# Performance work log

Measured on AMD Instinct MI355X. Metric: run time of the kernel, lower is better.

The kernel has to match this reference:

```python
import jax, jax.numpy as jnp
from jax import lax
import numpy as np

B, C, H, W = 4, 256, 64, 64
CQK = C // 8  # 32


def conv3x3(x, w, b):
    # x: [B,C_in,H,W], w: [C_out,C_in,3,3], b: [C_out]
    y = lax.conv_general_dilated(x, w, window_strides=(1, 1), padding='SAME',
                                 dimension_numbers=('NCHW', 'OIHW', 'NCHW'))
    return y + b[None, :, None, None]


def setup_inputs() -> dict:
    key = jax.random.key(0)
    ks = jax.random.split(key, 8)
    scale = 0.02
    return {
        'x': jax.random.normal(ks[0], (B, C, H, W), dtype=jnp.float32),
        'wq': jax.random.normal(ks[1], (CQK, C, 3, 3), dtype=jnp.float32) * scale,
        'bq': jax.random.normal(ks[2], (CQK,), dtype=jnp.float32) * scale,
        'wk': jax.random.normal(ks[3], (CQK, C, 3, 3), dtype=jnp.float32) * scale,
        'bk': jax.random.normal(ks[4], (CQK,), dtype=jnp.float32) * scale,
        'wv': jax.random.normal(ks[5], (C, C, 3, 3), dtype=jnp.float32) * scale,
        'bv': jax.random.normal(ks[6], (C,), dtype=jnp.float32) * scale,
        'gamma': jax.random.normal(ks[7], (1,), dtype=jnp.float32) * scale,
    }


def reference(x, wq, bq, wk, bk, wv, bv, gamma):
    b, c, h, w = x.shape
    n = h * w
    # Q: [B, N, C//8]  (permute(0,2,1) of the flattened conv output)
    q = conv3x3(x, wq, bq).reshape(b, -1, n).transpose(0, 2, 1)
    # K: [B, C//8, N]
    k = conv3x3(x, wk, bk).reshape(b, -1, n)
    # s: [B, N_q, N_k]
    s = jnp.einsum('bqd,bdk->bqk', q, k)
    # NOTE: original uses Softmax(dim=-2), i.e. over the QUERY axis
    attn_T = jax.nn.softmax(s, axis=-2)
    # V: [B, C, N]
    v = conv3x3(x, wv, bv).reshape(b, c, n)
    # o = bmm(V, attn_T): [B, C, N]
    o = jnp.einsum('bcq,bqk->bck', v, attn_T).reshape(b, c, h, w)
    return x + gamma * o
```

## Files before the change

kernel.cpp:

```cpp
#include <hip/hip_runtime.h>
#include <cstddef>

#define N_PIX 4096
#define HW 64
#define LOG2E 1.4426950408889634f
#define SHIFT2 28.8539008177793f

typedef __attribute__((ext_vector_type(8))) short bf16x8;
typedef __attribute__((ext_vector_type(4))) float f32x4;
typedef unsigned int u32;

static __device__ __forceinline__ unsigned short f2bf(float f) {
    union { float f; unsigned u; } v; v.f = f;
    unsigned r = v.u + 0x7fffu + ((v.u >> 16) & 1u);
    return (unsigned short)(r >> 16);
}
static __device__ __forceinline__ float bf2f(unsigned short s) {
    union { unsigned u; float f; } v; v.u = (unsigned)s << 16;
    return v.f;
}
static __device__ __forceinline__ unsigned pack_bf16_trunc(float lo, float hi) {
    union { float f; unsigned u; } a, b; a.f = hi; b.f = lo;
    return __builtin_amdgcn_perm(a.u, b.u, 0x07060302u);
}
static __device__ __forceinline__ void gll16(const void* g, void* l) {
    __builtin_amdgcn_global_load_lds(
        (const __attribute__((address_space(1))) u32*)g,
        (__attribute__((address_space(3))) u32*)l, 16, 0, 0);
}

__global__ __launch_bounds__(256) void x_transpose(
    const float* __restrict__ x, unsigned short* __restrict__ xbf)
{
    __shared__ unsigned short Ts[64][72];
    const int tid = threadIdx.x;
    const int px0 = blockIdx.x * 64, ci0 = blockIdx.y * 64, b = blockIdx.z;
    const float* xb = x + ((size_t)b * 256 + ci0) * N_PIX;

#pragma unroll
    for (int r = 0; r < 4; ++r) {
        int c = r * 16 + (tid >> 4);
        int p4 = (tid & 15) * 4;
        float4 v = *(const float4*)&xb[(size_t)c * N_PIX + px0 + p4];
        Ts[c][p4 + 0] = f2bf(v.x);
        Ts[c][p4 + 1] = f2bf(v.y);
        Ts[c][p4 + 2] = f2bf(v.z);
        Ts[c][p4 + 3] = f2bf(v.w);
    }
    __syncthreads();
#pragma unroll
    for (int r = 0; r < 2; ++r) {
        int id = tid * 2 + r;
        int p = id >> 3, c8 = (id & 7) * 8;
        ushort4 lo, hi;
        lo.x = Ts[c8 + 0][p]; lo.y = Ts[c8 + 1][p];
        lo.z = Ts[c8 + 2][p]; lo.w = Ts[c8 + 3][p];
        hi.x = Ts[c8 + 4][p]; hi.y = Ts[c8 + 5][p];
        hi.z = Ts[c8 + 6][p]; hi.w = Ts[c8 + 7][p];
        size_t off = ((size_t)b * N_PIX + px0 + p) * 256 + ci0 + c8;
        *(ushort4*)&xbf[off]     = lo;
        *(ushort4*)&xbf[off + 4] = hi;
    }
}

__global__ __launch_bounds__(256) void w_transform(
    const float* __restrict__ wq, const float* __restrict__ wk,
    const float* __restrict__ wv, unsigned short* __restrict__ wAll,
    unsigned short* __restrict__ zp)
{
    int gid = blockIdx.x * 256 + threadIdx.x;
    if (gid < 256) zp[gid] = 0;
    if (gid >= 72 * 320 * 4) return;
    int part = gid & 3;
    int m = (gid >> 2) % 320;
    int kb = gid / 1280;
    int t = kb >> 3;
    int ci0 = (kb & 7) * 32 + part * 8;
    const float* src; int co; float sc = 1.f;
    if (m < 256)      { src = wv; co = m; }
    else if (m < 288) { src = wq; co = m - 256; sc = LOG2E; }
    else              { src = wk; co = m - 288; }
    ushort4 lo, hi;
    lo.x = f2bf(sc * src[((size_t)co * 256 + ci0 + 0) * 9 + t]);
    lo.y = f2bf(sc * src[((size_t)co * 256 + ci0 + 1) * 9 + t]);
    lo.z = f2bf(sc * src[((size_t)co * 256 + ci0 + 2) * 9 + t]);
    lo.w = f2bf(sc * src[((size_t)co * 256 + ci0 + 3) * 9 + t]);
    hi.x = f2bf(sc * src[((size_t)co * 256 + ci0 + 4) * 9 + t]);
    hi.y = f2bf(sc * src[((size_t)co * 256 + ci0 + 5) * 9 + t]);
    hi.z = f2bf(sc * src[((size_t)co * 256 + ci0 + 6) * 9 + t]);
    hi.w = f2bf(sc * src[((size_t)co * 256 + ci0 + 7) * 9 + t]);
    size_t off = ((size_t)kb * 320 + m) * 32 + part * 8;
    *(ushort4*)&wAll[off]     = lo;
    *(ushort4*)&wAll[off + 4] = hi;
}

__global__ __launch_bounds__(256, 2) void conv_gemm_v6(
    const unsigned short* __restrict__ xbf, const unsigned short* __restrict__ wAll,
    const float* __restrict__ bq, const float* __restrict__ bk,
    const float* __restrict__ bv, const unsigned short* __restrict__ zpage,
    unsigned short* __restrict__ vbf, unsigned short* __restrict__ qt,
    unsigned short* __restrict__ kt)
{
    __shared__ unsigned short Bl[3 * 7168];

    const int tid = threadIdx.x;
    const int w = tid >> 6, lane = tid & 63, quad = lane >> 4, l15 = lane & 15;
    const int y = blockIdx.x, rh = blockIdx.y, b = blockIdx.z;
    const int rg = w >> 1;
    const int pxh = w & 1;

    const unsigned short* xb = xbf + (size_t)b * N_PIX * 256;
    const unsigned short* aSrc = wAll + (size_t)rh * 160 * 32;

    auto stage = [&](int kb, int buf) {
        const int t_ = kb >> 3;
        const int ty = t_ / 3;
        const int dy = ty - 1, dx = t_ - ty * 3 - 1;
        const int gy = y + dy;
        const bool rowOK = ((unsigned)gy < 64u);
        const int ci0 = (kb & 7) * 32;
        const unsigned short* aS = aSrc + (size_t)kb * 10240;
        unsigned short* tile = &Bl[buf * 7168];
#pragma unroll
        for (int r = 0; r < 4; ++r) {
            const int c = r * 4 + w;
            if (r == 3 && w >= 2) continue;
            if (c < 10) {
                int o = c * 1024 + lane * 16;
                int u = o ^ (((o >> 7) & 7) << 4);
                gll16(aS + (u >> 1), tile + c * 512);
            } else {
                int o = (c - 10) * 1024 + lane * 16;
                int u = o ^ (((o >> 7) & 7) << 4);
                int px = u >> 6, k16 = (u >> 4) & 3;
                int gx = px + dx;
                const unsigned short* src =
                    (rowOK && (unsigned)gx < 64u)
                        ? xb + ((size_t)(gy * 64 + gx) * 256 + ci0 + k16 * 8)
                        : zpage;
                gll16(src, tile + 5120 + (c - 10) * 512);
            }
        }
    };

    f32x4 acc[5][2];
#pragma unroll
    for (int cb = 0; cb < 5; ++cb)
#pragma unroll
        for (int jb = 0; jb < 2; ++jb) acc[cb][jb] = (f32x4){0.f, 0.f, 0.f, 0.f};

    stage(0, 0);
    stage(1, 1);
    if (w < 2) asm volatile("s_waitcnt vmcnt(4)" ::: "memory");
    else       asm volatile("s_waitcnt vmcnt(3)" ::: "memory");
    __builtin_amdgcn_s_barrier();
    __builtin_amdgcn_sched_barrier(0);

    int buf = 0;
    for (int kb = 0; kb < 72; ++kb) {
        int nb = buf + 1; if (nb == 3) nb = 0;
        int pb = nb + 1;  if (pb == 3) pb = 0;
        const bool more2 = (kb + 2 < 72);
        const bool more1 = (kb + 1 < 72);
        if (more2) stage(kb + 2, pb);

        const int bb = buf * 7168;
        bf16x8 af[5], bfr[2];
#pragma unroll
        for (int cb = 0; cb < 5; ++cb) {
            int sr = rg * 80 + cb * 16 + l15;
            int u = sr * 64 + quad * 16;
            u ^= ((u >> 7) & 7) << 4;
            af[cb] = *(const bf16x8*)&Bl[bb + (u >> 1)];
        }
#pragma unroll
        for (int jb = 0; jb < 2; ++jb) {
            int px = pxh * 32 + jb * 16 + l15;
            int u = px * 64 + quad * 16;
            u ^= ((u >> 7) & 7) << 4;
            bfr[jb] = *(const bf16x8*)&Bl[bb + 5120 + (u >> 1)];
        }
        __builtin_amdgcn_s_setprio(1);
#pragma unroll
        for (int cb = 0; cb < 5; ++cb)
#pragma unroll
            for (int jb = 0; jb < 2; ++jb)
                acc[cb][jb] = __builtin_amdgcn_mfma_f32_16x16x32_bf16(
                    af[cb], bfr[jb], acc[cb][jb], 0, 0, 0);
        __builtin_amdgcn_s_setprio(0);

        if (more2) {
            if (w < 2) asm volatile("s_waitcnt vmcnt(4)" ::: "memory");
            else       asm volatile("s_waitcnt vmcnt(3)" ::: "memory");
        } else if (more1) {
            asm volatile("s_waitcnt vmcnt(0)" ::: "memory");
        }
        if (more1) {
            __builtin_amdgcn_s_barrier();
            __builtin_amdgcn_sched_barrier(0);
        }
        buf = nb;
    }

#pragma unroll
    for (int cb = 0; cb < 5; ++cb) {
        int cBase = rh * 160 + rg * 80 + cb * 16 + quad * 4;
#pragma unroll
        for (int r = 0; r < 4; ++r) {
            int c = cBase + r;
            if (c < 256) {
                float bias = bv[c];
#pragma unroll
                for (int jb = 0; jb < 2; ++jb) {
                    int px = y * 64 + pxh * 32 + jb * 16 + l15;
                    vbf[((size_t)b * 256 + c) * N_PIX + px] = f2bf(acc[cb][jb][r] + bias);
                }
            } else if (c < 288) {
                float bias = bq[c - 256] * LOG2E;
#pragma unroll
                for (int jb = 0; jb < 2; ++jb) {
                    int px = y * 64 + pxh * 32 + jb * 16 + l15;
                    qt[((size_t)b * N_PIX + px) * 32 + (c - 256)] = f2bf(acc[cb][jb][r] + bias);
                }
            } else {
                float bias = bk[c - 288];
#pragma unroll
                for (int jb = 0; jb < 2; ++jb) {
                    int px = y * 64 + pxh * 32 + jb * 16 + l15;
                    kt[((size_t)b * N_PIX + px) * 32 + (c - 288)] = f2bf(acc[cb][jb][r] + bias);
                }
            }
        }
    }
}

__global__ __launch_bounds__(256, 2) void fused_attn_mfma(
    const unsigned short* __restrict__ qt, const unsigned short* __restrict__ kt,
    const unsigned short* __restrict__ vbf,
    unsigned short* __restrict__ Abuf, float* __restrict__ lbuf, int iRange)
{
    const int tid  = threadIdx.x;
    const int w    = tid >> 6;
    const int lane = tid & 63;
    const int quad = lane >> 4;
    const int l15  = lane & 15;
    const int j0   = blockIdx.x * 128;
    const int b    = blockIdx.y;
    const int sp   = blockIdx.z;
    const int iBeg = sp * iRange;
    const int NI   = iRange / 64;

    const unsigned short* qtb = qt + (size_t)b * N_PIX * 32;
    const unsigned short* ktb = kt + (size_t)b * N_PIX * 32;
    const unsigned short* vb  = vbf + (size_t)b * 256 * N_PIX;

    __shared__ unsigned Pfrag[2][4096];
    __shared__ float lred[4][128];

    bf16x8 kf[8];
#pragma unroll
    for (int jb = 0; jb < 8; ++jb)
        kf[jb] = *(const bf16x8*)&ktb[((size_t)(j0 + jb * 16 + l15)) * 32 + quad * 8];

    f32x4 acc[4][8];
#pragma unroll
    for (int cb = 0; cb < 4; ++cb)
#pragma unroll
        for (int jb = 0; jb < 8; ++jb)
            acc[cb][jb] = (f32x4){0.f, 0.f, 0.f, 0.f};

    float lpart[8] = {0.f, 0.f, 0.f, 0.f, 0.f, 0.f, 0.f, 0.f};

    const int wFrag = w >> 1;
    const int wL    = ((w & 1) << 5) + ((quad >> 1) << 4) + l15;
    const int wEl2  = (quad & 1) << 1;

    bf16x8 va[2][4];

    auto s_phase = [&](bf16x8 qa, int buf) {
#pragma unroll
        for (int jb = 0; jb < 8; ++jb) {
            f32x4 s = __builtin_amdgcn_mfma_f32_16x16x32_bf16(
                qa, kf[jb], (f32x4){-SHIFT2, -SHIFT2, -SHIFT2, -SHIFT2}, 0, 0, 0);
            float p0 = __builtin_amdgcn_exp2f(s[0]);
            float p1 = __builtin_amdgcn_exp2f(s[1]);
            float p2 = __builtin_amdgcn_exp2f(s[2]);
            float p3 = __builtin_amdgcn_exp2f(s[3]);
            lpart[jb] += (p0 + p1) + (p2 + p3);
            unsigned u0 = pack_bf16_trunc(p0, p1);
            unsigned u1 = pack_bf16_trunc(p2, p3);
            unsigned base = (((jb << 1) + wFrag) * 64 + wL) * 4 + wEl2;
            Pfrag[buf][base]     = u0;
            Pfrag[buf][base + 1] = u1;
        }
    };

    auto load_qa = [&](int i0) {
        return *(const bf16x8*)&qtb[((size_t)(i0 + w * 16 + l15)) * 32 + quad * 8];
    };
    auto load_va = [&](int i0) {
#pragma unroll
        for (int ks = 0; ks < 2; ++ks)
#pragma unroll
            for (int cb = 0; cb < 4; ++cb)
                va[ks][cb] = *(const bf16x8*)&vb[((size_t)(w * 64 + cb * 16 + l15)) * N_PIX
                                                 + i0 + ks * 32 + quad * 8];
    };

    load_va(iBeg);
    s_phase(load_qa(iBeg), 0);

    for (int n = 0; n < NI; ++n) {
        __syncthreads();
        const bool hasN = (n + 1 < NI);
        const int inext = iBeg + (n + 1) * 64;
        bf16x8 qaN;
        if (hasN) qaN = load_qa(inext);

#pragma unroll
        for (int ks = 0; ks < 2; ++ks) {
            bf16x8 pb[8];
#pragma unroll
            for (int jb = 0; jb < 8; ++jb)
                pb[jb] = *(const bf16x8*)&Pfrag[n & 1][(((jb << 1) + ks) * 64 + lane) * 4];
#pragma unroll
            for (int cb = 0; cb < 4; ++cb)
#pragma unroll
                for (int jb = 0; jb < 8; ++jb)
                    acc[cb][jb] = __builtin_amdgcn_mfma_f32_16x16x32_bf16(
                        va[ks][cb], pb[jb], acc[cb][jb], 0, 0, 0);
        }

        if (hasN) {
            load_va(inext);
            s_phase(qaN, (n + 1) & 1);
        }
    }

#pragma unroll
    for (int jb = 0; jb < 8; ++jb) {
        float v = lpart[jb];
        v += __shfl_xor(v, 16, 64);
        v += __shfl_xor(v, 32, 64);
        lpart[jb] = v;
    }
    if (lane < 16) {
#pragma unroll
        for (int jb = 0; jb < 8; ++jb)
            lred[w][jb * 16 + l15] = lpart[jb];
    }
    __syncthreads();
    if (tid < 128) {
        float s = lred[0][tid] + lred[1][tid] + lred[2][tid] + lred[3][tid];
        lbuf[((size_t)sp * 4 + b) * N_PIX + j0 + tid] = s;
    }

    unsigned short* Ab = Abuf + ((size_t)sp * 4 + b) * 256 * N_PIX;
#pragma unroll
    for (int cb = 0; cb < 4; ++cb) {
        int c = w * 64 + cb * 16 + quad * 4;
#pragma unroll
        for (int jb = 0; jb < 8; ++jb) {
            int j = j0 + jb * 16 + l15;
#pragma unroll
            for (int r = 0; r < 4; ++r)
                Ab[(size_t)(c + r) * N_PIX + j] = f2bf(acc[cb][jb][r]);
        }
    }
}

__global__ __launch_bounds__(256) void combine_kernel(
    const unsigned short* __restrict__ A, const float* __restrict__ L,
    const float* __restrict__ x, const float* __restrict__ gamma,
    float* __restrict__ out, int split)
{
    const size_t CH = (size_t)4 * 256 * N_PIX;
    size_t flat = ((size_t)blockIdx.x * 256 + threadIdx.x) * 8;
    int j = (int)(flat & (N_PIX - 1));
    int b = (int)(flat >> 20);

    float a[8] = {0.f, 0.f, 0.f, 0.f, 0.f, 0.f, 0.f, 0.f};
    float l[8] = {0.f, 0.f, 0.f, 0.f, 0.f, 0.f, 0.f, 0.f};
    for (int s = 0; s < split; ++s) {
        ushort4 av0 = *(const ushort4*)&A[flat + (size_t)s * CH];
        ushort4 av1 = *(const ushort4*)&A[flat + (size_t)s * CH + 4];
        a[0] += bf2f(av0.x); a[1] += bf2f(av0.y); a[2] += bf2f(av0.z); a[3] += bf2f(av0.w);
        a[4] += bf2f(av1.x); a[5] += bf2f(av1.y); a[6] += bf2f(av1.z); a[7] += bf2f(av1.w);
        float4 l0 = *(const float4*)&L[((size_t)s * 4 + b) * N_PIX + j];
        float4 l1 = *(const float4*)&L[((size_t)s * 4 + b) * N_PIX + j + 4];
        l[0] += l0.x; l[1] += l0.y; l[2] += l0.z; l[3] += l0.w;
        l[4] += l1.x; l[5] += l1.y; l[6] += l1.z; l[7] += l1.w;
    }
    float g = gamma[0];
    float4 x0 = *(const float4*)&x[flat];
    float4 x1 = *(const float4*)&x[flat + 4];
    float4 o0, o1;
    o0.x = x0.x + g * a[0] / l[0];
    o0.y = x0.y + g * a[1] / l[1];
    o0.z = x0.z + g * a[2] / l[2];
    o0.w = x0.w + g * a[3] / l[3];
    o1.x = x1.x + g * a[4] / l[4];
    o1.y = x1.y + g * a[5] / l[5];
    o1.z = x1.z + g * a[6] / l[6];
    o1.w = x1.w + g * a[7] / l[7];
    *(float4*)&out[flat]     = o0;
    *(float4*)&out[flat + 4] = o1;
}

extern "C" void kernel_launch(void* const* d_in, const int* in_sizes, int n_in,
                              void* d_out, int out_size, void* d_ws, size_t ws_size,
                              hipStream_t stream)
{
    const float* x     = (const float*)d_in[0];
    const float* wq    = (const float*)d_in[1];
    const float* bq    = (const float*)d_in[2];
    const float* wk    = (const float*)d_in[3];
    const float* bk    = (const float*)d_in[4];
    const float* wv    = (const float*)d_in[5];
    const float* bv    = (const float*)d_in[6];
    const float* gamma = (const float*)d_in[7];
    float* out = (float*)d_out;

    const size_t szQTel  = (size_t)4 * N_PIX * 32;
    const size_t szVBFel = (size_t)4 * 256 * N_PIX;
    const size_t szXBFel = (size_t)4 * N_PIX * 256;
    const size_t szWel   = (size_t)72 * 320 * 32;
    const size_t fixedB  = (2 * szQTel + szVBFel + szXBFel + szWel + 256) * 2;

    int split = 4;
    while (split > 1) {
        size_t need = fixedB
                    + (size_t)split * 4 * 256 * N_PIX * 2
                    + (size_t)split * 4 * N_PIX * 4;
        if (need <= ws_size) break;
        split >>= 1;
    }

    unsigned short* Abuf = (unsigned short*)d_ws;
    float* lbuf = (float*)(Abuf + (size_t)split * 4 * 256 * N_PIX);
    unsigned short* qt    = (unsigned short*)(lbuf + (size_t)split * 4 * N_PIX);
    unsigned short* kt    = qt + szQTel;
    unsigned short* vbf   = kt + szQTel;
    unsigned short* xbf   = vbf + szVBFel;
    unsigned short* wAll  = xbf + szXBFel;
    unsigned short* zpage = wAll + szWel;

    x_transpose<<<dim3(N_PIX / 64, 4, 4), 256, 0, stream>>>(x, xbf);
    w_transform<<<dim3((72 * 320 * 4 + 255) / 256), 256, 0, stream>>>(
        wq, wk, wv, wAll, zpage);

    conv_gemm_v6<<<dim3(HW, 2, 4), 256, 0, stream>>>(
        xbf, wAll, bq, bk, bv, zpage, vbf, qt, kt);

    fused_attn_mfma<<<dim3(N_PIX / 128, 4, split), 256, 0, stream>>>(
        qt, kt, vbf, Abuf, lbuf, N_PIX / split);

    combine_kernel<<<dim3((4 * 256 * N_PIX) / (256 * 8)), 256, 0, stream>>>(
        Abuf, lbuf, x, gamma, out, split);
}
```

Before: 178.7 us.

## Merge prep kernels, deepen conv pipeline to four stages, raise attention MFMA priority

Combines the x transpose and weight transform into one launch, using an extra grid slice for the weights to save a kernel launch. Deepens the conv GEMM LDS ring from three buffers to four so loads are issued three K-blocks ahead, with vmcnt waits adjusted for each tail stage. Also wraps the attention MFMA loop in s_setprio. The fourth buffer raises LDS use, which may reduce occupancy at two blocks per CU.

```diff
diff --git a/kernel.cpp b/kernel.cpp
--- a/kernel.cpp
+++ b/kernel.cpp
@@ -29,79 +29,82 @@
         (__attribute__((address_space(3))) u32*)l, 16, 0, 0);
 }
 
-__global__ __launch_bounds__(256) void x_transpose(
-    const float* __restrict__ x, unsigned short* __restrict__ xbf)
-{
-    __shared__ unsigned short Ts[64][72];
-    const int tid = threadIdx.x;
-    const int px0 = blockIdx.x * 64, ci0 = blockIdx.y * 64, b = blockIdx.z;
-    const float* xb = x + ((size_t)b * 256 + ci0) * N_PIX;
-
-#pragma unroll
-    for (int r = 0; r < 4; ++r) {
-        int c = r * 16 + (tid >> 4);
-        int p4 = (tid & 15) * 4;
-        float4 v = *(const float4*)&xb[(size_t)c * N_PIX + px0 + p4];
-        Ts[c][p4 + 0] = f2bf(v.x);
-        Ts[c][p4 + 1] = f2bf(v.y);
-        Ts[c][p4 + 2] = f2bf(v.z);
-        Ts[c][p4 + 3] = f2bf(v.w);
-    }
-    __syncthreads();
-#pragma unroll
-    for (int r = 0; r < 2; ++r) {
-        int id = tid * 2 + r;
-        int p = id >> 3, c8 = (id & 7) * 8;
-        ushort4 lo, hi;
-        lo.x = Ts[c8 + 0][p]; lo.y = Ts[c8 + 1][p];
-        lo.z = Ts[c8 + 2][p]; lo.w = Ts[c8 + 3][p];
-        hi.x = Ts[c8 + 4][p]; hi.y = Ts[c8 + 5][p];
-        hi.z = Ts[c8 + 6][p]; hi.w = Ts[c8 + 7][p];
-        size_t off = ((size_t)b * N_PIX + px0 + p) * 256 + ci0 + c8;
-        *(ushort4*)&xbf[off]     = lo;
-        *(ushort4*)&xbf[off + 4] = hi;
-    }
-}
-
-__global__ __launch_bounds__(256) void w_transform(
+__global__ __launch_bounds__(256) void prep_kernel(
+    const float* __restrict__ x, unsigned short* __restrict__ xbf,
     const float* __restrict__ wq, const float* __restrict__ wk,
     const float* __restrict__ wv, unsigned short* __restrict__ wAll,
     unsigned short* __restrict__ zp)
 {
-    int gid = blockIdx.x * 256 + threadIdx.x;
-    if (gid < 256) zp[gid] = 0;
-    if (gid >= 72 * 320 * 4) return;
-    int part = gid & 3;
-    int m = (gid >> 2) % 320;
-    int kb = gid / 1280;
-    int t = kb >> 3;
-    int ci0 = (kb & 7) * 32 + part * 8;
-    const float* src; int co; float sc = 1.f;
-    if (m < 256)      { src = wv; co = m; }
-    else if (m < 288) { src = wq; co = m - 256; sc = LOG2E; }
-    else              { src = wk; co = m - 288; }
-    ushort4 lo, hi;
-    lo.x = f2bf(sc * src[((size_t)co * 256 + ci0 + 0) * 9 + t]);
-    lo.y = f2bf(sc * src[((size_t)co * 256 + ci0 + 1) * 9 + t]);
-    lo.z = f2bf(sc * src[((size_t)co * 256 + ci0 + 2) * 9 + t]);
-    lo.w = f2bf(sc * src[((size_t)co * 256 + ci0 + 3) * 9 + t]);
-    hi.x = f2bf(sc * src[((size_t)co * 256 + ci0 + 4) * 9 + t]);
-    hi.y = f2bf(sc * src[((size_t)co * 256 + ci0 + 5) * 9 + t]);
-    hi.z = f2bf(sc * src[((size_t)co * 256 + ci0 + 6) * 9 + t]);
-    hi.w = f2bf(sc * src[((size_t)co * 256 + ci0 + 7) * 9 + t]);
-    size_t off = ((size_t)kb * 320 + m) * 32 + part * 8;
-    *(ushort4*)&wAll[off]     = lo;
-    *(ushort4*)&wAll[off + 4] = hi;
-}
-
-__global__ __launch_bounds__(256, 2) void conv_gemm_v6(
+    const int tid = threadIdx.x;
+    if (blockIdx.z < 4) {
+        __shared__ unsigned short Ts[64][72];
+        const int px0 = blockIdx.x * 64, ci0 = blockIdx.y * 64, b = blockIdx.z;
+        const float* xb = x + ((size_t)b * 256 + ci0) * N_PIX;
+
+#pragma unroll
+        for (int r = 0; r < 4; ++r) {
+            int c = r * 16 + (tid >> 4);
+            int p4 = (tid & 15) * 4;
+            float4 v = *(const float4*)&xb[(size_t)c * N_PIX + px0 + p4];
+            Ts[c][p4 + 0] = f2bf(v.x);
+            Ts[c][p4 + 1] = f2bf(v.y);
+            Ts[c][p4 + 2] = f2bf(v.z);
+            Ts[c][p4 + 3] = f2bf(v.w);
+        }
+        __syncthreads();
+#pragma unroll
+        for (int r = 0; r < 2; ++r) {
+            int id = tid * 2 + r;
+            int p = id >> 3, c8 = (id & 7) * 8;
+            ushort4 lo, hi;
+            lo.x = Ts[c8 + 0][p]; lo.y = Ts[c8 + 1][p];
+            lo.z = Ts[c8 + 2][p]; lo.w = Ts[c8 + 3][p];
+            hi.x = Ts[c8 + 4][p]; hi.y = Ts[c8 + 5][p];
+            hi.z = Ts[c8 + 6][p]; hi.w = Ts[c8 + 7][p];
+            size_t off = ((size_t)b * N_PIX + px0 + p) * 256 + ci0 + c8;
+            *(ushort4*)&xbf[off]     = lo;
+            *(ushort4*)&xbf[off + 4] = hi;
+        }
+    } else {
+        const int f = blockIdx.y * 64 + blockIdx.x;
+#pragma unroll
+        for (int base = 0; base < 2; ++base) {
+            int gid = base * 65536 + f * 256 + tid;
+            if (gid < 256) zp[gid] = 0;
+            if (gid >= 72 * 320 * 4) continue;
+            int part = gid & 3;
+            int m = (gid >> 2) % 320;
+            int kb = gid / 1280;
+            int t = kb >> 3;
+            int ci0 = (kb & 7) * 32 + part * 8;
+            const float* src; int co; float sc = 1.f;
+            if (m < 256)      { src = wv; co = m; }
+            else if (m < 288) { src = wq; co = m - 256; sc = LOG2E; }
+            else              { src = wk; co = m - 288; }
+            ushort4 lo, hi;
+            lo.x = f2bf(sc * src[((size_t)co * 256 + ci0 + 0) * 9 + t]);
+            lo.y = f2bf(sc * src[((size_t)co * 256 + ci0 + 1) * 9 + t]);
+            lo.z = f2bf(sc * src[((size_t)co * 256 + ci0 + 2) * 9 + t]);
+            lo.w = f2bf(sc * src[((size_t)co * 256 + ci0 + 3) * 9 + t]);
+            hi.x = f2bf(sc * src[((size_t)co * 256 + ci0 + 4) * 9 + t]);
+            hi.y = f2bf(sc * src[((size_t)co * 256 + ci0 + 5) * 9 + t]);
+            hi.z = f2bf(sc * src[((size_t)co * 256 + ci0 + 6) * 9 + t]);
+            hi.w = f2bf(sc * src[((size_t)co * 256 + ci0 + 7) * 9 + t]);
+            size_t off = ((size_t)kb * 320 + m) * 32 + part * 8;
+            *(ushort4*)&wAll[off]     = lo;
+            *(ushort4*)&wAll[off + 4] = hi;
+        }
+    }
+}
+
+__global__ __launch_bounds__(256, 2) void conv_gemm_v7(
     const unsigned short* __restrict__ xbf, const unsigned short* __restrict__ wAll,
     const float* __restrict__ bq, const float* __restrict__ bk,
     const float* __restrict__ bv, const unsigned short* __restrict__ zpage,
     unsigned short* __restrict__ vbf, unsigned short* __restrict__ qt,
     unsigned short* __restrict__ kt)
 {
-    __shared__ unsigned short Bl[3 * 7168];
+    __shared__ unsigned short Bl[4 * 7168];
 
     const int tid = threadIdx.x;
     const int w = tid >> 6, lane = tid & 63, quad = lane >> 4, l15 = lane & 15;
@@ -151,18 +154,15 @@
 
     stage(0, 0);
     stage(1, 1);
-    if (w < 2) asm volatile("s_waitcnt vmcnt(4)" ::: "memory");
-    else       asm volatile("s_waitcnt vmcnt(3)" ::: "memory");
+    stage(2, 2);
+    if (w < 2) asm volatile("s_waitcnt vmcnt(8)" ::: "memory");
+    else       asm volatile("s_waitcnt vmcnt(6)" ::: "memory");
     __builtin_amdgcn_s_barrier();
     __builtin_amdgcn_sched_barrier(0);
 
-    int buf = 0;
     for (int kb = 0; kb < 72; ++kb) {
-        int nb = buf + 1; if (nb == 3) nb = 0;
-        int pb = nb + 1;  if (pb == 3) pb = 0;
-        const bool more2 = (kb + 2 < 72);
-        const bool more1 = (kb + 1 < 72);
-        if (more2) stage(kb + 2, pb);
+        const int buf = kb & 3;
+        if (kb + 3 < 72) stage(kb + 3, (kb + 3) & 3);
 
         const int bb = buf * 7168;
         bf16x8 af[5], bfr[2];
@@ -189,17 +189,19 @@
                     af[cb], bfr[jb], acc[cb][jb], 0, 0, 0);
         __builtin_amdgcn_s_setprio(0);
 
-        if (more2) {
+        if (kb + 3 < 72) {
+            if (w < 2) asm volatile("s_waitcnt vmcnt(8)" ::: "memory");
+            else       asm volatile("s_waitcnt vmcnt(6)" ::: "memory");
+        } else if (kb + 2 < 72) {
             if (w < 2) asm volatile("s_waitcnt vmcnt(4)" ::: "memory");
             else       asm volatile("s_waitcnt vmcnt(3)" ::: "memory");
-        } else if (more1) {
+        } else if (kb + 1 < 72) {
             asm volatile("s_waitcnt vmcnt(0)" ::: "memory");
         }
-        if (more1) {
+        if (kb + 1 < 72) {
             __builtin_amdgcn_s_barrier();
             __builtin_amdgcn_sched_barrier(0);
         }
-        buf = nb;
     }
 
 #pragma unroll
@@ -323,12 +325,14 @@
 #pragma unroll
             for (int jb = 0; jb < 8; ++jb)
                 pb[jb] = *(const bf16x8*)&Pfrag[n & 1][(((jb << 1) + ks) * 64 + lane) * 4];
+            __builtin_amdgcn_s_setprio(1);
 #pragma unroll
             for (int cb = 0; cb < 4; ++cb)
 #pragma unroll
                 for (int jb = 0; jb < 8; ++jb)
                     acc[cb][jb] = __builtin_amdgcn_mfma_f32_16x16x32_bf16(
                         va[ks][cb], pb[jb], acc[cb][jb], 0, 0, 0);
+            __builtin_amdgcn_s_setprio(0);
         }
 
         if (hasN) {
@@ -445,11 +449,10 @@
     unsigned short* wAll  = xbf + szXBFel;
     unsigned short* zpage = wAll + szWel;
 
-    x_transpose<<<dim3(N_PIX / 64, 4, 4), 256, 0, stream>>>(x, xbf);
-    w_transform<<<dim3((72 * 320 * 4 + 255) / 256), 256, 0, stream>>>(
-        wq, wk, wv, wAll, zpage);
-
-    conv_gemm_v6<<<dim3(HW, 2, 4), 256, 0, stream>>>(
+    prep_kernel<<<dim3(N_PIX / 64, 4, 5), 256, 0, stream>>>(
+        x, xbf, wq, wk, wv, wAll, zpage);
+
+    conv_gemm_v7<<<dim3(HW, 2, 4), 256, 0, stream>>>(
         xbf, wAll, bq, bk, bv, zpage, vbf, qt, kt);
 
     fused_attn_mfma<<<dim3(N_PIX / 128, 4, split), 256, 0, stream>>>(
```

New measurement: 179.2 us. Within noise of the previous version (+0.3%).
